# Kernel optimization log

Measured on AMD Instinct MI355X. Metric: run time of the kernel, lower is better.

The kernel has to match this reference:

```python
import jax, jax.numpy as jnp
import numpy as np

N_NODES = 50000
N_EDGES = 200000
D_FEAT = 512
D_HID = 1024


def setup_inputs() -> dict:
    key = jax.random.key(0)
    k_x, k_s, k_d, k_w1, k_w2 = jax.random.split(key, 5)
    x = jax.random.normal(k_x, (N_NODES, D_FEAT), dtype=jnp.float32)
    src = jax.random.randint(k_s, (N_EDGES,), 0, N_NODES, dtype=jnp.int64)
    dst = jax.random.randint(k_d, (N_EDGES,), 0, N_NODES, dtype=jnp.int64)
    # MLP params: Linear(2d -> hidden), ReLU, Linear(hidden -> 1)
    W1 = jax.random.normal(k_w1, (2 * D_FEAT, D_HID), dtype=jnp.float32) * (1.0 / np.sqrt(2 * D_FEAT))
    b1 = jnp.zeros((D_HID,), dtype=jnp.float32)
    W2 = jax.random.normal(k_w2, (D_HID, 1), dtype=jnp.float32) * (1.0 / np.sqrt(D_HID))
    b2 = jnp.zeros((1,), dtype=jnp.float32)
    return {"x": x, "src": src, "dst": dst, "W1": W1, "b1": b1, "W2": W2, "b2": b2}


def reference(x, src, dst, W1, b1, W2, b2):
    # Per-edge gather of src/dst node embeddings, concat along feature dim
    h = jnp.concatenate([x[src], x[dst]], axis=1)          # [E, 2d]
    h = jax.nn.relu(h @ W1 + b1)                            # [E, hidden]
    score = h @ W2 + b2                                     # [E, 1]
    return score
```

## Files before the change

kernel.cpp:

```cpp
#include <hip/hip_runtime.h>
#include <cstdint>
#include <cstddef>

typedef __attribute__((ext_vector_type(8))) short short8;
typedef __attribute__((ext_vector_type(4))) float f32x4;

#define D_FEAT 512
#define D_HID  1024
#define NCOL   2048
#define NCHUNK 32

__device__ __forceinline__ unsigned short f2bf(float f) {
    unsigned u = __builtin_bit_cast(unsigned, f);
    u += 0x7FFFu + ((u >> 16) & 1u);
    return (unsigned short)(u >> 16);
}

__global__ __launch_bounds__(256) void cast_x_kernel(const float* __restrict__ x,
                                                     unsigned short* __restrict__ xb,
                                                     int n) {
    int i = (blockIdx.x * 256 + threadIdx.x) * 8;
    if (i >= n) return;
    const float4* xp = (const float4*)(x + i);
    float4 a = xp[0], b = xp[1];
    short8 o;
    o[0] = (short)f2bf(a.x); o[1] = (short)f2bf(a.y);
    o[2] = (short)f2bf(a.z); o[3] = (short)f2bf(a.w);
    o[4] = (short)f2bf(b.x); o[5] = (short)f2bf(b.y);
    o[6] = (short)f2bf(b.z); o[7] = (short)f2bf(b.w);
    *(short8*)(xb + i) = o;
}

__global__ __launch_bounds__(256) void transpose_w1_kernel(const float* __restrict__ W1,
                                                           unsigned short* __restrict__ w1t) {
    __shared__ float tile[32][33];
    const int half = blockIdx.z;
    const int kb = blockIdx.y * 32;
    const int nb = blockIdx.x * 32;
    const int tx = threadIdx.x, ty = threadIdx.y;
    #pragma unroll
    for (int i = 0; i < 32; i += 8)
        tile[ty + i][tx] = W1[(size_t)(half * 512 + kb + ty + i) * 1024 + nb + tx];
    __syncthreads();
    #pragma unroll
    for (int i = 0; i < 32; i += 8)
        w1t[(size_t)(half * 1024 + nb + ty + i) * 512 + kb + tx] = f2bf(tile[tx][ty + i]);
}

#define BM 128
#define BN 128
#define BK 64
#define GM 32

__global__ __launch_bounds__(256, 2) void gemm_uv_kernel(
    const unsigned short* __restrict__ xb,
    const unsigned short* __restrict__ w1t,
    const float* __restrict__ b1,
    unsigned char* __restrict__ qUV,
    float* __restrict__ scales,
    int M, int MB)
{
    __shared__ __align__(16) unsigned short smem[16384];
    unsigned short* sA = smem;
    unsigned short* sB = smem + 8192;

    const int NB = NCOL / BN;
    int bid = blockIdx.x;
    int g    = bid / (GM * NB);
    int rem  = bid - g * (GM * NB);
    int base = g * GM;
    int gm   = MB - base; if (gm > GM) gm = GM;
    int mb   = base + rem % gm;
    int nb   = rem / gm;
    const int m0 = mb * BM;
    const int n0 = nb * BN;

    const int tid  = threadIdx.x;
    const int wave = tid >> 6;
    const int lane = tid & 63;
    const int q    = lane >> 4;
    const int l15  = lane & 15;
    const int wm   = (wave >> 1) * 64;
    const int wn   = (wave & 1) * 64;

    const int ar = lane >> 3;
    const int ac = ((lane & 7) ^ ar) * 8;

    const int swz = l15 & 7;
    const int c0 = (q ^ swz) * 8;
    const int c1 = ((q ^ swz) ^ 4) * 8;

    float b1v[4];
    #pragma unroll
    for (int nt = 0; nt < 4; ++nt) {
        int n = n0 + wn + nt * 16 + l15;
        b1v[nt] = (n < D_HID) ? b1[n] : 0.f;
    }

    f32x4 acc[4][4];
    #pragma unroll
    for (int i = 0; i < 4; ++i)
        #pragma unroll
        for (int j = 0; j < 4; ++j)
            acc[i][j] = (f32x4){b1v[j], b1v[j], b1v[j], b1v[j]};

    #pragma unroll 1
    for (int kt = 0; kt < 8; ++kt) {
        const int k0 = kt * BK;
        __syncthreads();
        #pragma unroll
        for (int i = 0; i < 4; ++i) {
            int slot = wave * 4 + i;
            int row  = slot * 8 + ar;
            int m    = m0 + row; if (m >= M) m = M - 1;
            __builtin_amdgcn_global_load_lds(
                (const __attribute__((address_space(1))) void*)(xb + (size_t)m * D_FEAT + k0 + ac),
                (__attribute__((address_space(3))) void*)(sA + slot * 512),
                16, 0, 0);
        }
        #pragma unroll
        for (int i = 0; i < 4; ++i) {
            int slot = wave * 4 + i;
            int row  = slot * 8 + ar;
            __builtin_amdgcn_global_load_lds(
                (const __attribute__((address_space(1))) void*)(w1t + (size_t)(n0 + row) * D_FEAT + k0 + ac),
                (__attribute__((address_space(3))) void*)(sB + slot * 512),
                16, 0, 0);
        }
        __syncthreads();
        {
            short8 a[4], b[4];
            #pragma unroll
            for (int mt = 0; mt < 4; ++mt)
                a[mt] = *(const short8*)(sA + (wm + mt * 16 + l15) * 64 + c0);
            #pragma unroll
            for (int nt = 0; nt < 4; ++nt)
                b[nt] = *(const short8*)(sB + (wn + nt * 16 + l15) * 64 + c0);
            #pragma unroll
            for (int mt = 0; mt < 4; ++mt)
                #pragma unroll
                for (int nt = 0; nt < 4; ++nt)
                    acc[mt][nt] = __builtin_amdgcn_mfma_f32_16x16x32_bf16(a[mt], b[nt], acc[mt][nt], 0, 0, 0);
            #pragma unroll
            for (int mt = 0; mt < 4; ++mt)
                a[mt] = *(const short8*)(sA + (wm + mt * 16 + l15) * 64 + c1);
            #pragma unroll
            for (int nt = 0; nt < 4; ++nt)
                b[nt] = *(const short8*)(sB + (wn + nt * 16 + l15) * 64 + c1);
            #pragma unroll
            for (int mt = 0; mt < 4; ++mt)
                #pragma unroll
                for (int nt = 0; nt < 4; ++nt)
                    acc[mt][nt] = __builtin_amdgcn_mfma_f32_16x16x32_bf16(a[mt], b[nt], acc[mt][nt], 0, 0, 0);
        }
    }

    float msc[4], minv[4];
    #pragma unroll
    for (int mt = 0; mt < 4; ++mt) {
        float m_ = 1e-30f;
        #pragma unroll
        for (int nt = 0; nt < 4; ++nt)
            #pragma unroll
            for (int r = 0; r < 4; ++r)
                m_ = fmaxf(m_, fabsf(acc[mt][nt][r]));
        #pragma unroll
        for (int off = 1; off < 64; off <<= 1)
            m_ = fmaxf(m_, __shfl_xor(m_, off));
        msc[mt]  = m_ * (1.0f / 127.0f);
        minv[mt] = 127.0f * __builtin_amdgcn_rcpf(m_);
    }

    __syncthreads();
    unsigned char* ep8 = (unsigned char*)smem + wave * 4096;
    const float MAGIC = 12583040.0f;
    #pragma unroll
    for (int mt = 0; mt < 4; ++mt)
        #pragma unroll
        for (int nt = 0; nt < 4; ++nt)
            #pragma unroll
            for (int r = 0; r < 4; ++r) {
                float f = fmaf(acc[mt][nt][r], minv[mt], MAGIC);
                ep8[(mt * 16 + q * 4 + r) * 64 + nt * 16 + l15] =
                    (unsigned char)__builtin_bit_cast(unsigned, f);
            }
    const int chunk = (n0 + wn) >> 6;
    {
        int srow = m0 + wm + q * 16 + l15;
        if (srow < M) scales[(size_t)srow * NCHUNK + chunk] = msc[q];
    }
    #pragma unroll
    for (int i = 0; i < 4; ++i) {
        int flat = i * 64 + lane;
        int r   = flat >> 2;
        int c16 = (flat & 3) * 16;
        int m   = m0 + wm + r;
        if (m < M) {
            int4 v = *(const int4*)(ep8 + r * 64 + c16);
            *(int4*)(qUV + (size_t)m * NCOL + n0 + wn + c16) = v;
        }
    }
}

__global__ __launch_bounds__(256) void edge_score_kernel(
    const unsigned char* __restrict__ qUV,
    const float* __restrict__ scales,
    const int* __restrict__ src, const int* __restrict__ dst,
    const float* __restrict__ W2, const float* __restrict__ b2,
    float* __restrict__ out, int E)
{
    const int wave = threadIdx.x >> 6;
    const int lane = threadIdx.x & 63;
    const int gw = blockIdx.x * 4 + wave;
    const int e0 = gw * 2;
    const int e1 = e0 + 1;
    if (e0 >= E) return;
    const bool has1 = (e1 < E);

    const int s0 = src[e0];
    const int d0 = dst[e0];
    const int s1 = has1 ? src[e1] : s0;
    const int d1 = has1 ? dst[e1] : d0;

    uint4 qu0 = *(const uint4*)(qUV + (size_t)s0 * NCOL + lane * 16);
    uint4 qv0 = *(const uint4*)(qUV + (size_t)d0 * NCOL + D_HID + lane * 16);
    uint4 qu1 = *(const uint4*)(qUV + (size_t)s1 * NCOL + lane * 16);
    uint4 qv1 = *(const uint4*)(qUV + (size_t)d1 * NCOL + D_HID + lane * 16);
    const int ch = lane >> 2;
    float su0 = scales[(size_t)s0 * NCHUNK + ch];
    float sv0 = scales[(size_t)d0 * NCHUNK + 16 + ch];
    float su1 = scales[(size_t)s1 * NCHUNK + ch];
    float sv1 = scales[(size_t)d1 * NCHUNK + 16 + ch];
    float cc0 = -128.0f * (su0 + sv0);
    float cc1 = -128.0f * (su1 + sv1);

    const float4* wp = (const float4*)(W2 + lane * 16);
    float4 wa = wp[0], wb = wp[1], wc = wp[2], wd = wp[3];
    float w[16] = {wa.x, wa.y, wa.z, wa.w, wb.x, wb.y, wb.z, wb.w,
                   wc.x, wc.y, wc.z, wc.w, wd.x, wd.y, wd.z, wd.w};
    const float bias = b2[0];

    const unsigned* u0w = (const unsigned*)&qu0; const unsigned* v0w = (const unsigned*)&qv0;
    const unsigned* u1w = (const unsigned*)&qu1; const unsigned* v1w = (const unsigned*)&qv1;

    float acc0 = 0.f, acc1 = 0.f;
    #pragma unroll
    for (int dw = 0; dw < 4; ++dw) {
        #pragma unroll
        for (int b = 0; b < 4; ++b) {
            int k = dw * 4 + b;
            float ub0 = (float)((u0w[dw] >> (8 * b)) & 0xFFu);
            float vb0 = (float)((v0w[dw] >> (8 * b)) & 0xFFu);
            float h0 = fmaf(ub0, su0, fmaf(vb0, sv0, cc0));
            acc0 = fmaf(fmaxf(h0, 0.f), w[k], acc0);
            float ub1 = (float)((u1w[dw] >> (8 * b)) & 0xFFu);
            float vb1 = (float)((v1w[dw] >> (8 * b)) & 0xFFu);
            float h1 = fmaf(ub1, su1, fmaf(vb1, sv1, cc1));
            acc1 = fmaf(fmaxf(h1, 0.f), w[k], acc1);
        }
    }
    #pragma unroll
    for (int off = 1; off < 64; off <<= 1) {
        acc0 += __shfl_xor(acc0, off);
        acc1 += __shfl_xor(acc1, off);
    }
    if (lane == 0) out[e0] = acc0 + bias;
    if (lane == 1 && has1) out[e1] = acc1 + bias;
}

extern "C" void kernel_launch(void* const* d_in, const int* in_sizes, int n_in,
                              void* d_out, int out_size, void* d_ws, size_t ws_size,
                              hipStream_t stream) {
    const float* x   = (const float*)d_in[0];
    const int*   src = (const int*)d_in[1];
    const int*   dst = (const int*)d_in[2];
    const float* W1  = (const float*)d_in[3];
    const float* b1  = (const float*)d_in[4];
    const float* W2  = (const float*)d_in[5];
    const float* b2  = (const float*)d_in[6];
    float* out = (float*)d_out;

    const int M = in_sizes[0] / D_FEAT;
    const int E = in_sizes[1];

    char* ws = (char*)d_ws;
    unsigned char*  qUV    = (unsigned char*)ws;
    float*          scales = (float*)(ws + (size_t)M * NCOL);
    unsigned short* xb     = (unsigned short*)(ws + (size_t)M * NCOL + (size_t)M * NCHUNK * 4);
    unsigned short* w1t    = (unsigned short*)(ws + (size_t)M * NCOL + (size_t)M * NCHUNK * 4
                                                  + (size_t)M * D_FEAT * 2);

    const int nx = M * D_FEAT;
    cast_x_kernel<<<(nx / 8 + 255) / 256, 256, 0, stream>>>(x, xb, nx);
    transpose_w1_kernel<<<dim3(32, 16, 2), dim3(32, 8), 0, stream>>>(W1, w1t);
    const int MB = (M + BM - 1) / BM;
    gemm_uv_kernel<<<MB * (NCOL / BN), 256, 0, stream>>>(xb, w1t, b1, qUV, scales, M, MB);
    edge_score_kernel<<<(E + 7) / 8, 256, 0, stream>>>(qUV, scales, src, dst, W2, b2, out, E);
}
```

Measured before the change: 342.4 us.

## Enlarge GEMM tiles to 256x256 with double-buffered LDS and split-phase MFMA pipeline

The node-projection GEMM moves from 128x128 tiles with 4 waves to 256x256 tiles with 8 waves. LDS buffers are double-buffered so the next k-tile's A and B loads overlap the MFMA phases, and s_setprio raises wave priority during compute. The epilogue swizzles its LDS layout to reduce bank conflicts. This costs 128KB of LDS and more registers per thread, fewer blocks in flight, and tail waste when M is not a multiple of 256.

```diff
diff --git a/kernel.cpp b/kernel.cpp
--- a/kernel.cpp
+++ b/kernel.cpp
@@ -15,6 +15,9 @@
     u += 0x7FFFu + ((u >> 16) & 1u);
     return (unsigned short)(u >> 16);
 }
+
+#define FENCE() asm volatile("" ::: "memory")
+#define BAR()   do { FENCE(); __builtin_amdgcn_s_barrier(); FENCE(); } while (0)
 
 __global__ __launch_bounds__(256) void cast_x_kernel(const float* __restrict__ x,
                                                      unsigned short* __restrict__ xb,
@@ -47,12 +50,13 @@
         w1t[(size_t)(half * 1024 + nb + ty + i) * 512 + kb + tx] = f2bf(tile[tx][ty + i]);
 }
 
-#define BM 128
-#define BN 128
+#define BM 256
+#define BN 256
 #define BK 64
 #define GM 32
-
-__global__ __launch_bounds__(256, 2) void gemm_uv_kernel(
+#define NB2 (NCOL / BN)
+
+__global__ __launch_bounds__(512, 2) void gemm_uv_kernel(
     const unsigned short* __restrict__ xb,
     const unsigned short* __restrict__ w1t,
     const float* __restrict__ b1,
@@ -60,14 +64,11 @@
     float* __restrict__ scales,
     int M, int MB)
 {
-    __shared__ __align__(16) unsigned short smem[16384];
-    unsigned short* sA = smem;
-    unsigned short* sB = smem + 8192;
-
-    const int NB = NCOL / BN;
-    int bid = blockIdx.x;
-    int g    = bid / (GM * NB);
-    int rem  = bid - g * (GM * NB);
+    __shared__ __align__(16) unsigned short smem[65536];
+
+    const int bid = blockIdx.x;
+    int g    = bid / (GM * NB2);
+    int rem  = bid - g * (GM * NB2);
     int base = g * GM;
     int gm   = MB - base; if (gm > GM) gm = GM;
     int mb   = base + rem % gm;
@@ -80,84 +81,140 @@
     const int lane = tid & 63;
     const int q    = lane >> 4;
     const int l15  = lane & 15;
-    const int wm   = (wave >> 1) * 64;
-    const int wn   = (wave & 1) * 64;
-
-    const int ar = lane >> 3;
-    const int ac = ((lane & 7) ^ ar) * 8;
-
-    const int swz = l15 & 7;
-    const int c0 = (q ^ swz) * 8;
-    const int c1 = ((q ^ swz) ^ 4) * 8;
+    const int wr   = wave >> 2;
+    const int wc   = wave & 3;
+    const int bh   = wc >> 1;
+
+    const int ar    = lane >> 3;
+    const int swcol = ((lane & 7) ^ ar) * 8;
+    const int swz   = l15 & 7;
+
+    const int slotA0 = wr * 16 + wc * 4;
+    const int slotB0 = bh * 16 + (wr * 2 + (wc & 1)) * 4;
+    int rowA[4], rowB[4];
+    #pragma unroll
+    for (int j = 0; j < 4; ++j) {
+        int m = m0 + (slotA0 + j) * 8 + ar;
+        rowA[j] = (m < M) ? m : (M - 1);
+        rowB[j] = n0 + (slotB0 + j) * 8 + ar;
+    }
+
+    unsigned short* const sAbuf[2] = { smem,         smem + 16384 };
+    unsigned short* const sBbuf[2] = { smem + 32768, smem + 49152 };
+
+    auto stageA = [&](int t, int cb) {
+        const int k0 = t * BK;
+        #pragma unroll
+        for (int j = 0; j < 4; ++j)
+            __builtin_amdgcn_global_load_lds(
+                (const __attribute__((address_space(1))) void*)(xb + ((size_t)rowA[j] << 9) + k0 + swcol),
+                (__attribute__((address_space(3))) void*)(sAbuf[cb] + (slotA0 + j) * 512),
+                16, 0, 0);
+    };
+    auto stageB = [&](int t, int cb) {
+        const int k0 = t * BK;
+        #pragma unroll
+        for (int j = 0; j < 4; ++j)
+            __builtin_amdgcn_global_load_lds(
+                (const __attribute__((address_space(1))) void*)(w1t + ((size_t)rowB[j] << 9) + k0 + swcol),
+                (__attribute__((address_space(3))) void*)(sBbuf[cb] + (slotB0 + j) * 512),
+                16, 0, 0);
+    };
+    auto readA = [&](int cb, int mt, int ks) -> short8 {
+        int row = wr * 128 + mt * 16 + l15;
+        return *(const short8*)(sAbuf[cb] + row * 64 + (((q | (ks << 2)) ^ swz) * 8));
+    };
+    auto readB = [&](int cb, int nt, int ks) -> short8 {
+        int row = wc * 64 + nt * 16 + l15;
+        return *(const short8*)(sBbuf[cb] + row * 64 + (((q | (ks << 2)) ^ swz) * 8));
+    };
 
     float b1v[4];
     #pragma unroll
     for (int nt = 0; nt < 4; ++nt) {
-        int n = n0 + wn + nt * 16 + l15;
+        int n = n0 + wc * 64 + nt * 16 + l15;
         b1v[nt] = (n < D_HID) ? b1[n] : 0.f;
     }
-
-    f32x4 acc[4][4];
-    #pragma unroll
-    for (int i = 0; i < 4; ++i)
+    f32x4 acc[8][4];
+    #pragma unroll
+    for (int i = 0; i < 8; ++i)
         #pragma unroll
         for (int j = 0; j < 4; ++j)
             acc[i][j] = (f32x4){b1v[j], b1v[j], b1v[j], b1v[j]};
 
-    #pragma unroll 1
-    for (int kt = 0; kt < 8; ++kt) {
-        const int k0 = kt * BK;
-        __syncthreads();
-        #pragma unroll
-        for (int i = 0; i < 4; ++i) {
-            int slot = wave * 4 + i;
-            int row  = slot * 8 + ar;
-            int m    = m0 + row; if (m >= M) m = M - 1;
-            __builtin_amdgcn_global_load_lds(
-                (const __attribute__((address_space(1))) void*)(xb + (size_t)m * D_FEAT + k0 + ac),
-                (__attribute__((address_space(3))) void*)(sA + slot * 512),
-                16, 0, 0);
-        }
-        #pragma unroll
-        for (int i = 0; i < 4; ++i) {
-            int slot = wave * 4 + i;
-            int row  = slot * 8 + ar;
-            __builtin_amdgcn_global_load_lds(
-                (const __attribute__((address_space(1))) void*)(w1t + (size_t)(n0 + row) * D_FEAT + k0 + ac),
-                (__attribute__((address_space(3))) void*)(sB + slot * 512),
-                16, 0, 0);
-        }
-        __syncthreads();
-        {
-            short8 a[4], b[4];
-            #pragma unroll
-            for (int mt = 0; mt < 4; ++mt)
-                a[mt] = *(const short8*)(sA + (wm + mt * 16 + l15) * 64 + c0);
+    stageA(0, 0);
+    stageB(0, 0);
+    asm volatile("s_waitcnt vmcnt(0)" ::: "memory");
+    BAR();
+
+    #pragma unroll
+    for (int t = 0; t < 8; ++t) {
+        const int c = t & 1;
+        short8 a[4], bk0[4], bk1[4];
+
+        #pragma unroll
+        for (int nt = 0; nt < 4; ++nt) bk0[nt] = readB(c, nt, 0);
+        #pragma unroll
+        for (int i = 0; i < 4; ++i)    a[i]    = readA(c, i, 0);
+        if (t < 7) stageA(t + 1, c ^ 1);
+        BAR();
+        asm volatile("s_waitcnt lgkmcnt(0)" ::: "memory");
+        __builtin_amdgcn_s_setprio(1);
+        #pragma unroll
+        for (int mt = 0; mt < 4; ++mt)
             #pragma unroll
             for (int nt = 0; nt < 4; ++nt)
-                b[nt] = *(const short8*)(sB + (wn + nt * 16 + l15) * 64 + c0);
-            #pragma unroll
-            for (int mt = 0; mt < 4; ++mt)
-                #pragma unroll
-                for (int nt = 0; nt < 4; ++nt)
-                    acc[mt][nt] = __builtin_amdgcn_mfma_f32_16x16x32_bf16(a[mt], b[nt], acc[mt][nt], 0, 0, 0);
-            #pragma unroll
-            for (int mt = 0; mt < 4; ++mt)
-                a[mt] = *(const short8*)(sA + (wm + mt * 16 + l15) * 64 + c1);
+                acc[mt][nt] = __builtin_amdgcn_mfma_f32_16x16x32_bf16(a[mt], bk0[nt], acc[mt][nt], 0, 0, 0);
+        __builtin_amdgcn_s_setprio(0);
+        BAR();
+
+        #pragma unroll
+        for (int nt = 0; nt < 4; ++nt) bk1[nt] = readB(c, nt, 1);
+        #pragma unroll
+        for (int i = 0; i < 4; ++i)    a[i]    = readA(c, i, 1);
+        if (t < 7) stageB(t + 1, c ^ 1);
+        BAR();
+        asm volatile("s_waitcnt lgkmcnt(0)" ::: "memory");
+        __builtin_amdgcn_s_setprio(1);
+        #pragma unroll
+        for (int mt = 0; mt < 4; ++mt)
             #pragma unroll
             for (int nt = 0; nt < 4; ++nt)
-                b[nt] = *(const short8*)(sB + (wn + nt * 16 + l15) * 64 + c1);
-            #pragma unroll
-            for (int mt = 0; mt < 4; ++mt)
-                #pragma unroll
-                for (int nt = 0; nt < 4; ++nt)
-                    acc[mt][nt] = __builtin_amdgcn_mfma_f32_16x16x32_bf16(a[mt], b[nt], acc[mt][nt], 0, 0, 0);
-        }
-    }
-
-    float msc[4], minv[4];
-    #pragma unroll
-    for (int mt = 0; mt < 4; ++mt) {
+                acc[mt][nt] = __builtin_amdgcn_mfma_f32_16x16x32_bf16(a[mt], bk1[nt], acc[mt][nt], 0, 0, 0);
+        __builtin_amdgcn_s_setprio(0);
+        BAR();
+
+        #pragma unroll
+        for (int i = 0; i < 4; ++i) a[i] = readA(c, 4 + i, 0);
+        BAR();
+        asm volatile("s_waitcnt lgkmcnt(0)" ::: "memory");
+        __builtin_amdgcn_s_setprio(1);
+        #pragma unroll
+        for (int mt = 0; mt < 4; ++mt)
+            #pragma unroll
+            for (int nt = 0; nt < 4; ++nt)
+                acc[4 + mt][nt] = __builtin_amdgcn_mfma_f32_16x16x32_bf16(a[mt], bk0[nt], acc[4 + mt][nt], 0, 0, 0);
+        __builtin_amdgcn_s_setprio(0);
+        BAR();
+
+        #pragma unroll
+        for (int i = 0; i < 4; ++i) a[i] = readA(c, 4 + i, 1);
+        BAR();
+        asm volatile("s_waitcnt lgkmcnt(0)" ::: "memory");
+        __builtin_amdgcn_s_setprio(1);
+        #pragma unroll
+        for (int mt = 0; mt < 4; ++mt)
+            #pragma unroll
+            for (int nt = 0; nt < 4; ++nt)
+                acc[4 + mt][nt] = __builtin_amdgcn_mfma_f32_16x16x32_bf16(a[mt], bk1[nt], acc[4 + mt][nt], 0, 0, 0);
+        __builtin_amdgcn_s_setprio(0);
+        if (t < 7) asm volatile("s_waitcnt vmcnt(0)" ::: "memory");
+        BAR();
+    }
+
+    float msc[8], minv[8];
+    #pragma unroll
+    for (int mt = 0; mt < 8; ++mt) {
         float m_ = 1e-30f;
         #pragma unroll
         for (int nt = 0; nt < 4; ++nt)
@@ -171,33 +228,33 @@
         minv[mt] = 127.0f * __builtin_amdgcn_rcpf(m_);
     }
 
-    __syncthreads();
-    unsigned char* ep8 = (unsigned char*)smem + wave * 4096;
+    unsigned char* ep8 = (unsigned char*)smem + wave * 8192;
     const float MAGIC = 12583040.0f;
     #pragma unroll
-    for (int mt = 0; mt < 4; ++mt)
+    for (int mt = 0; mt < 8; ++mt)
         #pragma unroll
         for (int nt = 0; nt < 4; ++nt)
             #pragma unroll
             for (int r = 0; r < 4; ++r) {
                 float f = fmaf(acc[mt][nt][r], minv[mt], MAGIC);
-                ep8[(mt * 16 + q * 4 + r) * 64 + nt * 16 + l15] =
+                ep8[(mt * 16 + q * 4 + r) * 64 + ((nt ^ q) * 16) + l15] =
                     (unsigned char)__builtin_bit_cast(unsigned, f);
             }
-    const int chunk = (n0 + wn) >> 6;
-    {
-        int srow = m0 + wm + q * 16 + l15;
-        if (srow < M) scales[(size_t)srow * NCHUNK + chunk] = msc[q];
-    }
-    #pragma unroll
-    for (int i = 0; i < 4; ++i) {
-        int flat = i * 64 + lane;
+    const int chunk = (n0 + wc * 64) >> 6;
+    #pragma unroll
+    for (int h = 0; h < 2; ++h) {
+        int srow = m0 + wr * 128 + h * 64 + q * 16 + l15;
+        if (srow < M) scales[(size_t)srow * NCHUNK + chunk] = msc[h * 4 + q];
+    }
+    #pragma unroll
+    for (int it = 0; it < 8; ++it) {
+        int flat = it * 64 + lane;
         int r   = flat >> 2;
-        int c16 = (flat & 3) * 16;
-        int m   = m0 + wm + r;
+        int cI  = flat & 3;
+        int m   = m0 + wr * 128 + r;
         if (m < M) {
-            int4 v = *(const int4*)(ep8 + r * 64 + c16);
-            *(int4*)(qUV + (size_t)m * NCOL + n0 + wn + c16) = v;
+            int4 v = *(const int4*)(ep8 + r * 64 + ((cI ^ ((r >> 2) & 3)) * 16));
+            *(int4*)(qUV + (size_t)m * NCOL + n0 + wc * 64 + cI * 16) = v;
         }
     }
 }
@@ -294,6 +351,6 @@
     cast_x_kernel<<<(nx / 8 + 255) / 256, 256, 0, stream>>>(x, xb, nx);
     transpose_w1_kernel<<<dim3(32, 16, 2), dim3(32, 8), 0, stream>>>(W1, w1t);
     const int MB = (M + BM - 1) / BM;
-    gemm_uv_kernel<<<MB * (NCOL / BN), 256, 0, stream>>>(xb, w1t, b1, qUV, scales, M, MB);
+    gemm_uv_kernel<<<MB * NB2, 512, 0, stream>>>(xb, w1t, b1, qUV, scales, M, MB);
     edge_score_kernel<<<(E + 7) / 8, 256, 0, stream>>>(qUV, scales, src, dst, W2, b2, out, E);
 }
```

Result: slower. 365.8 us (+6.8%).
